# Kernel tuning notes

Measured on AMD Instinct MI355X. Metric: run time of the kernel, lower is better.

The kernel has to match this reference:

```python
import jax, jax.numpy as jnp
import numpy as np

D_MODEL = 1024
NUM_HEADS = 16
D_K = D_MODEL // NUM_HEADS


def setup_inputs() -> dict:
    key = jax.random.key(0)
    ks = jax.random.split(key, 11)
    B, T = 4, 2048
    s = 1.0 / np.sqrt(D_MODEL)
    inp = {
        "query": jax.random.normal(ks[0], (B, T, D_MODEL), jnp.float32),
        "key": jax.random.normal(ks[1], (B, T, D_MODEL), jnp.float32),
        "value": jax.random.normal(ks[2], (B, T, D_MODEL), jnp.float32),
        "Wq": jax.random.uniform(ks[3], (D_MODEL, D_MODEL), jnp.float32, -s, s),
        "bq": jax.random.uniform(ks[4], (D_MODEL,), jnp.float32, -s, s),
        "Wk": jax.random.uniform(ks[5], (D_MODEL, D_MODEL), jnp.float32, -s, s),
        "bk": jax.random.uniform(ks[6], (D_MODEL,), jnp.float32, -s, s),
        "Wv": jax.random.uniform(ks[7], (D_MODEL, D_MODEL), jnp.float32, -s, s),
        "bv": jax.random.uniform(ks[8], (D_MODEL,), jnp.float32, -s, s),
        "Wo": jax.random.uniform(ks[9], (D_MODEL, D_MODEL), jnp.float32, -s, s),
        "bo": jax.random.uniform(ks[10], (D_MODEL,), jnp.float32, -s, s),
    }
    return inp


def _split_heads(x):
    B, T, _ = x.shape
    return x.reshape(B, T, NUM_HEADS, D_K).transpose(0, 2, 1, 3)  # (B,H,T,dk)


def reference(query, key, value, Wq, bq, Wk, bk, Wv, bv, Wo, bo):
    q = _split_heads(query @ Wq + bq)   # (B,H,Tq,dk)
    k = _split_heads(key @ Wk + bk)     # (B,H,Tk,dk)
    v = _split_heads(value @ Wv + bv)   # (B,H,Tk,dk)
    scale = 1.0 / jnp.sqrt(jnp.asarray(D_K, q.dtype))
    scores = jnp.einsum("bhqd,bhkd->bhqk", q, k) * scale
    weights = jax.nn.softmax(scores, axis=-1)
    attn = jnp.einsum("bhqk,bhkd->bhqd", weights, v)  # (B,H,Tq,dk)
    B, H, T, dk = attn.shape
    attn = attn.transpose(0, 2, 1, 3).reshape(B, T, H * dk)
    return attn @ Wo + bo
```

## Files before the change

### kernel.cpp

```cpp
#include <hip/hip_runtime.h>
#include <hip/hip_bf16.h>
#include <stdint.h>


typedef __bf16 bf16x8 __attribute__((ext_vector_type(8)));
typedef float  f32x4  __attribute__((ext_vector_type(4)));

#define LOG2E 1.44269504088896340736f

static __device__ __forceinline__ uint32_t f2bf(float x) {
  uint32_t u = __float_as_uint(x);
  u += 0x7fffu + ((u >> 16) & 1u);
  return u >> 16;
}
#if __has_builtin(__builtin_amdgcn_cvt_pk_bf16_f32)
static __device__ __forceinline__ uint32_t pk2bf(float a, float b) {
  typedef __bf16 b2 __attribute__((ext_vector_type(2)));
  union { b2 v; uint32_t u; } x;
  x.v = __builtin_amdgcn_cvt_pk_bf16_f32(a, b);
  return x.u;
}
#else
static __device__ __forceinline__ uint32_t pk2bf(float a, float b) {
  return f2bf(a) | (f2bf(b) << 16);
}
#endif
static __device__ __forceinline__ void gl2lds16(const void* g, void* l) {
  __builtin_amdgcn_global_load_lds(
      (const __attribute__((address_space(1))) uint32_t*)g,
      (__attribute__((address_space(3))) uint32_t*)l, 16, 0, 0);
}

__global__ void transpose_weights(const float* __restrict__ Wq, const float* __restrict__ Wk,
                                  const float* __restrict__ Wv, const float* __restrict__ Wo,
                                  uint16_t* __restrict__ out) {
  __shared__ float t[32][33];
  const float* W = blockIdx.z == 0 ? Wq : blockIdx.z == 1 ? Wk : blockIdx.z == 2 ? Wv : Wo;
  uint16_t* O = out + (size_t)blockIdx.z * 1048576;
  int tx = threadIdx.x & 31, ty = threadIdx.x >> 5;
  int r0 = blockIdx.y * 32, c0 = blockIdx.x * 32;
#pragma unroll
  for (int i = 0; i < 4; i++) t[ty + i * 8][tx] = W[(size_t)(r0 + ty + i * 8) * 1024 + c0 + tx];
  __syncthreads();
#pragma unroll
  for (int i = 0; i < 4; i++)
    O[(size_t)(c0 + ty + i * 8) * 1024 + r0 + tx] = (uint16_t)f2bf(t[tx][ty + i * 8]);
}

template <bool AF32>
static __device__ __forceinline__ void gemm_body(
    const void* __restrict__ Ain, const uint16_t* __restrict__ Bt,
    const float* __restrict__ bias, void* __restrict__ Cout,
    int N, int K, int mode, float oscale, int mBase, int nBase,
    uint16_t* __restrict__ lA, uint16_t* __restrict__ lB) {
  int tid = threadIdx.x, wave = tid >> 6, lane = tid & 63;
  int q = lane >> 4, c = lane & 15;
  int wrow = wave & 1, wcol = wave >> 1;
  f32x4 acc[4][4] = {};

  int rho = lane >> 3, j = lane & 7;
  int swz = (j ^ rho) * 8;
  const uint16_t* gB  = Bt + (size_t)(nBase + wave * 32 + rho) * K + swz;
  const uint16_t* gA16 = (const uint16_t*)Ain + (size_t)(mBase + wave * 32 + rho) * K + swz;
  const float*    gA32 = (const float*)Ain + (size_t)(mBase + wave * 32 + rho) * K + swz;
  int cs = c & 7;

  for (int kt = 0; kt < K / 64; kt++) {
    __syncthreads();
    int k0 = kt * 64;
#pragma unroll
    for (int it = 0; it < 4; it++)
      gl2lds16(gB + (size_t)(it * 8) * K + k0, &lB[(wave * 32 + it * 8) * 64]);
    if (AF32) {
#pragma unroll
      for (int h2 = 0; h2 < 2; h2++) {
        float4 fa[2][2];
#pragma unroll
        for (int it = 0; it < 2; it++) {
          const float* p = gA32 + (size_t)((h2 * 2 + it) * 8) * K + k0;
          fa[it][0] = *(const float4*)p;
          fa[it][1] = *(const float4*)(p + 4);
        }
#pragma unroll
        for (int it = 0; it < 2; it++) {
          uint4 ov;
          ov.x = pk2bf(fa[it][0].x, fa[it][0].y);
          ov.y = pk2bf(fa[it][0].z, fa[it][0].w);
          ov.z = pk2bf(fa[it][1].x, fa[it][1].y);
          ov.w = pk2bf(fa[it][1].z, fa[it][1].w);
          *(uint4*)&lA[(wave * 32 + (h2 * 2 + it) * 8 + rho) * 64 + j * 8] = ov;
        }
      }
    } else {
#pragma unroll
      for (int it = 0; it < 4; it++)
        gl2lds16(gA16 + (size_t)(it * 8) * K + k0, &lA[(wave * 32 + it * 8) * 64]);
    }
    __syncthreads();
#pragma unroll
    for (int kk = 0; kk < 2; kk++) {
      bf16x8 af[4], bfr[4];
#pragma unroll
      for (int i = 0; i < 4; i++)
        af[i] = *(const bf16x8*)&lA[(wrow * 64 + i * 16 + c) * 64 + ((kk * 4 + q) ^ cs) * 8];
#pragma unroll
      for (int jj = 0; jj < 4; jj++)
        bfr[jj] = *(const bf16x8*)&lB[(wcol * 64 + jj * 16 + c) * 64 + ((kk * 4 + q) ^ cs) * 8];
#pragma unroll
      for (int i = 0; i < 4; i++)
#pragma unroll
        for (int jj = 0; jj < 4; jj++)
          acc[i][jj] = __builtin_amdgcn_mfma_f32_16x16x32_bf16(af[i], bfr[jj], acc[i][jj], 0, 0, 0);
    }
  }

  float bb[4];
#pragma unroll
  for (int jj = 0; jj < 4; jj++) bb[jj] = bias[nBase + wcol * 64 + jj * 16 + c];

  if (mode == 0) {
    float* Co = (float*)Cout;
#pragma unroll
    for (int i = 0; i < 4; i++)
#pragma unroll
      for (int jj = 0; jj < 4; jj++) {
        int row = mBase + wrow * 64 + i * 16 + q * 4;
        int col = nBase + wcol * 64 + jj * 16 + c;
#pragma unroll
        for (int r = 0; r < 4; r++) Co[(size_t)(row + r) * N + col] = acc[i][jj][r] + bb[jj];
      }
  } else if (mode == 1) {
    uint16_t* Co = (uint16_t*)Cout;
#pragma unroll
    for (int i = 0; i < 4; i++)
#pragma unroll
      for (int jj = 0; jj < 4; jj++) {
        int row = mBase + wrow * 64 + i * 16 + q * 4;
        int col = nBase + wcol * 64 + jj * 16 + c;
#pragma unroll
        for (int r = 0; r < 4; r++)
          Co[(size_t)(row + r) * N + col] = (uint16_t)f2bf((acc[i][jj][r] + bb[jj]) * oscale);
      }
  } else {
    uint16_t* Co = (uint16_t*)Cout;
#pragma unroll
    for (int i = 0; i < 4; i++)
#pragma unroll
      for (int jj = 0; jj < 4; jj++) {
        int n = nBase + wcol * 64 + jj * 16 + c;
        int h = n >> 6, d = n & 63;
        int m = mBase + wrow * 64 + i * 16 + q * 4;
        int b = m >> 11, t = m & 2047;
        uint32_t lo = pk2bf(acc[i][jj][0] + bb[jj], acc[i][jj][1] + bb[jj]);
        uint32_t hi = pk2bf(acc[i][jj][2] + bb[jj], acc[i][jj][3] + bb[jj]);
        *(uint2*)(Co + (size_t)((b * 16 + h) * 64 + d) * 2048 + t) = make_uint2(lo, hi);
      }
  }
}

__global__ __launch_bounds__(256, 2)
void gemm_qkv(const float* __restrict__ qs, const float* __restrict__ ks,
              const float* __restrict__ vs, const uint16_t* __restrict__ Wtq,
              const uint16_t* __restrict__ Wtk, const uint16_t* __restrict__ Wtv,
              const float* __restrict__ bq, const float* __restrict__ bk,
              const float* __restrict__ bv, uint16_t* __restrict__ Qp,
              uint16_t* __restrict__ Kp, uint16_t* __restrict__ Vt, float cs) {
  __shared__ uint16_t lA[8192], lB[8192];
  int id = blockIdx.x + (blockIdx.y << 3) + (blockIdx.z << 9);
  int xcd = id & 7, j = id >> 3;
  int bx = j & 7;
  int by = xcd * 8 + ((j >> 3) & 7);
  int z  = j >> 6;
  const void* A      = z == 0 ? (const void*)qs : (z == 1 ? (const void*)ks : (const void*)vs);
  const uint16_t* Bt = z == 0 ? Wtq : (z == 1 ? Wtk : Wtv);
  const float* bias  = z == 0 ? bq : (z == 1 ? bk : bv);
  void* C            = z == 0 ? (void*)Qp : (z == 1 ? (void*)Kp : (void*)Vt);
  int mode   = z == 2 ? 2 : 1;
  float os   = z == 0 ? cs : 1.0f;
  gemm_body<true>(A, Bt, bias, C, 1024, 1024, mode, os, by * 128, bx * 128, lA, lB);
}

__global__ __launch_bounds__(256, 2)
void gemm_out(const uint16_t* __restrict__ A, const uint16_t* __restrict__ Bt,
              const float* __restrict__ bias, float* __restrict__ C) {
  __shared__ uint16_t lA[8192], lB[8192];
  int id = blockIdx.x + (blockIdx.y << 3);
  int xcd = id & 7, j = id >> 3;
  int bx = j & 7;
  int by = xcd * 8 + (j >> 3);
  gemm_body<false>(A, Bt, bias, C, 1024, 1024, 0, 1.0f, by * 128, bx * 128, lA, lB);
}

__global__ __launch_bounds__(256, 2)
void attn(const uint16_t* __restrict__ Qp, const uint16_t* __restrict__ Kp,
          const uint16_t* __restrict__ Vt, uint16_t* __restrict__ Ob) {
  __shared__ uint16_t lds[16384];
  int tid = threadIdx.x, wave = tid >> 6, lane = tid & 63;
  int q = lane >> 4, c = lane & 15;
  int cs = c & 7;
  int gq   = (c & 3) | (((c >> 2) & 1) << 2);
  int rowA = ((c >> 2) << 3) + (c & 3);

  int id = blockIdx.y * 16 + blockIdx.x;
  int wk = (id & 7) * 128 + (id >> 3);
  int qt = wk & 15, bh = wk >> 4;
  int b = bh >> 4, h = bh & 15;
  int qbase = qt * 128;
  int swz = ((lane & 7) ^ (lane >> 3)) * 8;

  {
    const uint16_t* gQ =
        Qp + (size_t)(b * 2048 + qbase + wave * 32 + (lane >> 3)) * 1024 + h * 64 + swz;
#pragma unroll
    for (int it = 0; it < 4; it++)
      gl2lds16(gQ + (size_t)(it * 8) * 1024, &lds[(wave * 32 + it * 8) * 64]);
  }
  __syncthreads();
  bf16x8 qf[2][2];
#pragma unroll
  for (int it = 0; it < 2; it++)
#pragma unroll
    for (int kk = 0; kk < 2; kk++)
      qf[it][kk] =
          *(const bf16x8*)&lds[(wave * 32 + it * 16 + c) * 64 + ((kk * 4 + q) ^ cs) * 8];
  __syncthreads();

  f32x4 o[4][2] = {};
  f32x4 lacc[2] = {};
  union { uint32_t u[4]; bf16x8 v; } one8;
  one8.u[0] = one8.u[1] = one8.u[2] = one8.u[3] = 0x3F803F80u;

  int kchunk = (lane & 7) ^ ((lane >> 3) & 3);
  const uint16_t* gKa =
      Kp + (size_t)(b * 2048 + wave * 16 + (lane >> 3)) * 1024 + h * 64 + kchunk * 8;
  const uint16_t* gKb =
      Kp + (size_t)(b * 2048 + wave * 16 + 8 + (lane >> 3)) * 1024 + h * 64 + (kchunk ^ 4) * 8;
  const uint16_t* gV0 = Vt + (size_t)(bh * 64 + wave * 16 + (lane >> 3)) * 2048 + swz;

  auto stage = [&](int tile, int nb) {
    gl2lds16(gKa + (size_t)(tile * 64) * 1024, &lds[nb + (wave * 16) * 64]);
    gl2lds16(gKb + (size_t)(tile * 64) * 1024, &lds[nb + (wave * 16 + 8) * 64]);
    gl2lds16(gV0 + (size_t)(tile * 64), &lds[8192 + nb + (wave * 16) * 64]);
    gl2lds16(gV0 + (size_t)(8 * 2048) + tile * 64, &lds[8192 + nb + (wave * 16 + 8) * 64]);
  };

  auto compute = [&](const uint16_t* sKc, const uint16_t* sVc) {
    f32x4 s[2][2][2];
#pragma unroll
    for (int p = 0; p < 2; p++) {
      const uint16_t* kr = &sKc[(p * 32 + rowA) * 64];
      bf16x8 aA0 = *(const bf16x8*)&kr[(q ^ gq) * 8];
      bf16x8 aA1 = *(const bf16x8*)&kr[((4 + q) ^ gq) * 8];
      bf16x8 aB0 = *(const bf16x8*)&kr[256 + (q ^ gq) * 8];
      bf16x8 aB1 = *(const bf16x8*)&kr[256 + ((4 + q) ^ gq) * 8];
      s[p][0][0] = __builtin_amdgcn_mfma_f32_16x16x32_bf16(aA0, qf[0][0],
                                                           (f32x4){0.f, 0.f, 0.f, 0.f}, 0, 0, 0);
      s[p][0][0] = __builtin_amdgcn_mfma_f32_16x16x32_bf16(aA1, qf[0][1], s[p][0][0], 0, 0, 0);
      s[p][0][1] = __builtin_amdgcn_mfma_f32_16x16x32_bf16(aA0, qf[1][0],
                                                           (f32x4){0.f, 0.f, 0.f, 0.f}, 0, 0, 0);
      s[p][0][1] = __builtin_amdgcn_mfma_f32_16x16x32_bf16(aA1, qf[1][1], s[p][0][1], 0, 0, 0);
      s[p][1][0] = __builtin_amdgcn_mfma_f32_16x16x32_bf16(aB0, qf[0][0],
                                                           (f32x4){0.f, 0.f, 0.f, 0.f}, 0, 0, 0);
      s[p][1][0] = __builtin_amdgcn_mfma_f32_16x16x32_bf16(aB1, qf[0][1], s[p][1][0], 0, 0, 0);
      s[p][1][1] = __builtin_amdgcn_mfma_f32_16x16x32_bf16(aB0, qf[1][0],
                                                           (f32x4){0.f, 0.f, 0.f, 0.f}, 0, 0, 0);
      s[p][1][1] = __builtin_amdgcn_mfma_f32_16x16x32_bf16(aB1, qf[1][1], s[p][1][1], 0, 0, 0);
    }
#pragma unroll
    for (int p = 0; p < 2; p++) {
      union { uint32_t u[4]; bf16x8 v; } pb[2];
#pragma unroll
      for (int it = 0; it < 2; it++) {
        float a0 = __builtin_amdgcn_exp2f(s[p][0][it][0]);
        float a1 = __builtin_amdgcn_exp2f(s[p][0][it][1]);
        float a2 = __builtin_amdgcn_exp2f(s[p][0][it][2]);
        float a3 = __builtin_amdgcn_exp2f(s[p][0][it][3]);
        float b0 = __builtin_amdgcn_exp2f(s[p][1][it][0]);
        float b1 = __builtin_amdgcn_exp2f(s[p][1][it][1]);
        float b2 = __builtin_amdgcn_exp2f(s[p][1][it][2]);
        float b3 = __builtin_amdgcn_exp2f(s[p][1][it][3]);
        pb[it].u[0] = pk2bf(a0, a1); pb[it].u[1] = pk2bf(a2, a3);
        pb[it].u[2] = pk2bf(b0, b1); pb[it].u[3] = pk2bf(b2, b3);
      }
      lacc[0] = __builtin_amdgcn_mfma_f32_16x16x32_bf16(one8.v, pb[0].v, lacc[0], 0, 0, 0);
      lacc[1] = __builtin_amdgcn_mfma_f32_16x16x32_bf16(one8.v, pb[1].v, lacc[1], 0, 0, 0);
#pragma unroll
      for (int mt = 0; mt < 4; mt++) {
        bf16x8 vv = *(const bf16x8*)&sVc[(mt * 16 + c) * 64 + (((p * 4 + q) ^ cs) * 8)];
        o[mt][0] = __builtin_amdgcn_mfma_f32_16x16x32_bf16(vv, pb[0].v, o[mt][0], 0, 0, 0);
        o[mt][1] = __builtin_amdgcn_mfma_f32_16x16x32_bf16(vv, pb[1].v, o[mt][1], 0, 0, 0);
      }
    }
  };

  stage(0, 0);
  for (int kt2 = 0; kt2 < 16; kt2++) {
    __syncthreads();
    stage(kt2 * 2 + 1, 4096);
    compute(&lds[0], &lds[8192]);
    __syncthreads();
    if (kt2 < 15) stage(kt2 * 2 + 2, 0);
    compute(&lds[4096], &lds[12288]);
  }

  float l[2] = {lacc[0][0], lacc[1][0]};

#pragma unroll
  for (int it = 0; it < 2; it++) {
    float inv = 1.0f / l[it];
    size_t trow = (size_t)(b * 2048 + qbase + wave * 32 + it * 16 + c) * 1024 + h * 64;
#pragma unroll
    for (int mt = 0; mt < 4; mt++) {
      uint32_t lo = pk2bf(o[mt][it][0] * inv, o[mt][it][1] * inv);
      uint32_t hi = pk2bf(o[mt][it][2] * inv, o[mt][it][3] * inv);
      *(uint2*)(Ob + trow + mt * 16 + q * 4) = make_uint2(lo, hi);
    }
  }
}

extern "C" void kernel_launch(void* const* d_in, const int* in_sizes, int n_in,
                              void* d_out, int out_size, void* d_ws, size_t ws_size,
                              hipStream_t stream) {
  (void)in_sizes; (void)n_in; (void)out_size; (void)ws_size;
  const float* query = (const float*)d_in[0];
  const float* key_  = (const float*)d_in[1];
  const float* value = (const float*)d_in[2];
  const float* Wq = (const float*)d_in[3]; const float* bq = (const float*)d_in[4];
  const float* Wk = (const float*)d_in[5]; const float* bk = (const float*)d_in[6];
  const float* Wv = (const float*)d_in[7]; const float* bv = (const float*)d_in[8];
  const float* Wo = (const float*)d_in[9]; const float* bo = (const float*)d_in[10];

  const size_t SZ = (size_t)8192 * 1024;
  uint16_t* buf0 = (uint16_t*)d_ws;
  uint16_t* buf1 = buf0 + SZ;
  uint16_t* buf2 = buf1 + SZ;
  uint16_t* buf3 = buf2 + SZ;
  uint16_t* wts  = buf3 + SZ;
  uint16_t* Wtq = wts;
  uint16_t* Wtk = wts + 1048576;
  uint16_t* Wtv = wts + 2097152;
  uint16_t* Wto = wts + 3145728;
  uint16_t* Kp  = wts + 4194304;
  uint16_t* Vt  = Kp + SZ;

  const float Cs = 0.125f * LOG2E;

  transpose_weights<<<dim3(32, 32, 4), 256, 0, stream>>>(Wq, Wk, Wv, Wo, wts);
  gemm_qkv<<<dim3(8, 64, 3), 256, 0, stream>>>(query, key_, value, Wtq, Wtk, Wtv,
                                               bq, bk, bv, buf3, Kp, Vt, Cs);
  attn<<<dim3(16, 64), 256, 0, stream>>>(buf3, Kp, Vt, buf2);
  gemm_out<<<dim3(8, 64), 256, 0, stream>>>(buf2, Wto, bo, (float*)d_out);
}
```

Baseline: 372.7 us.

## Double-buffer GEMM LDS tiles to overlap global loads with MFMA compute

Reworks the shared GEMM main loop into a two-stage ping-pong pipeline. The next K-tile's global loads (direct-to-LDS for bf16, register-staged for fp32 with bf16 conversion) are issued before computing on the current buffer, which hides load latency behind MFMA work. LDS per block doubles to 64 KB, and more fp32 staging registers stay live, both of which may reduce occupancy. The loop now hardcodes K/64 = 16 iterations.

```diff
diff --git a/kernel.cpp b/kernel.cpp
--- a/kernel.cpp
+++ b/kernel.cpp
@@ -60,58 +60,76 @@
 
   int rho = lane >> 3, j = lane & 7;
   int swz = (j ^ rho) * 8;
-  const uint16_t* gB  = Bt + (size_t)(nBase + wave * 32 + rho) * K + swz;
+  const uint16_t* gB   = Bt + (size_t)(nBase + wave * 32 + rho) * K + swz;
   const uint16_t* gA16 = (const uint16_t*)Ain + (size_t)(mBase + wave * 32 + rho) * K + swz;
   const float*    gA32 = (const float*)Ain + (size_t)(mBase + wave * 32 + rho) * K + swz;
   int cs = c & 7;
 
-  for (int kt = 0; kt < K / 64; kt++) {
-    __syncthreads();
-    int k0 = kt * 64;
+  float4 fa[4][2];
+
+  auto issueA32 = [&](int kt) {
+#pragma unroll
+    for (int it = 0; it < 4; it++) {
+      const float* p = gA32 + (size_t)(it * 8) * K + kt * 64;
+      fa[it][0] = *(const float4*)p;
+      fa[it][1] = *(const float4*)(p + 4);
+    }
+  };
+  auto writeA32 = [&](int nb) {
+#pragma unroll
+    for (int it = 0; it < 4; it++) {
+      uint4 ov;
+      ov.x = pk2bf(fa[it][0].x, fa[it][0].y);
+      ov.y = pk2bf(fa[it][0].z, fa[it][0].w);
+      ov.z = pk2bf(fa[it][1].x, fa[it][1].y);
+      ov.w = pk2bf(fa[it][1].z, fa[it][1].w);
+      *(uint4*)&lA[nb + (wave * 32 + it * 8 + rho) * 64 + j * 8] = ov;
+    }
+  };
+  auto issueA16 = [&](int kt, int nb) {
 #pragma unroll
     for (int it = 0; it < 4; it++)
-      gl2lds16(gB + (size_t)(it * 8) * K + k0, &lB[(wave * 32 + it * 8) * 64]);
-    if (AF32) {
-#pragma unroll
-      for (int h2 = 0; h2 < 2; h2++) {
-        float4 fa[2][2];
-#pragma unroll
-        for (int it = 0; it < 2; it++) {
-          const float* p = gA32 + (size_t)((h2 * 2 + it) * 8) * K + k0;
-          fa[it][0] = *(const float4*)p;
-          fa[it][1] = *(const float4*)(p + 4);
-        }
-#pragma unroll
-        for (int it = 0; it < 2; it++) {
-          uint4 ov;
-          ov.x = pk2bf(fa[it][0].x, fa[it][0].y);
-          ov.y = pk2bf(fa[it][0].z, fa[it][0].w);
-          ov.z = pk2bf(fa[it][1].x, fa[it][1].y);
-          ov.w = pk2bf(fa[it][1].z, fa[it][1].w);
-          *(uint4*)&lA[(wave * 32 + (h2 * 2 + it) * 8 + rho) * 64 + j * 8] = ov;
-        }
-      }
-    } else {
-#pragma unroll
-      for (int it = 0; it < 4; it++)
-        gl2lds16(gA16 + (size_t)(it * 8) * K + k0, &lA[(wave * 32 + it * 8) * 64]);
-    }
-    __syncthreads();
+      gl2lds16(gA16 + (size_t)(it * 8) * K + kt * 64, &lA[nb + (wave * 32 + it * 8) * 64]);
+  };
+  auto issueB = [&](int kt, int nb) {
+#pragma unroll
+    for (int it = 0; it < 4; it++)
+      gl2lds16(gB + (size_t)(it * 8) * K + kt * 64, &lB[nb + (wave * 32 + it * 8) * 64]);
+  };
+  auto compute = [&](int nb) {
 #pragma unroll
     for (int kk = 0; kk < 2; kk++) {
       bf16x8 af[4], bfr[4];
 #pragma unroll
       for (int i = 0; i < 4; i++)
-        af[i] = *(const bf16x8*)&lA[(wrow * 64 + i * 16 + c) * 64 + ((kk * 4 + q) ^ cs) * 8];
+        af[i] = *(const bf16x8*)&lA[nb + (wrow * 64 + i * 16 + c) * 64 + ((kk * 4 + q) ^ cs) * 8];
 #pragma unroll
       for (int jj = 0; jj < 4; jj++)
-        bfr[jj] = *(const bf16x8*)&lB[(wcol * 64 + jj * 16 + c) * 64 + ((kk * 4 + q) ^ cs) * 8];
+        bfr[jj] = *(const bf16x8*)&lB[nb + (wcol * 64 + jj * 16 + c) * 64 + ((kk * 4 + q) ^ cs) * 8];
 #pragma unroll
       for (int i = 0; i < 4; i++)
 #pragma unroll
         for (int jj = 0; jj < 4; jj++)
           acc[i][jj] = __builtin_amdgcn_mfma_f32_16x16x32_bf16(af[i], bfr[jj], acc[i][jj], 0, 0, 0);
     }
+  };
+
+  if (AF32) { issueA32(0); writeA32(0); } else issueA16(0, 0);
+  issueB(0, 0);
+
+  for (int kt2 = 0; kt2 < 8; kt2++) {
+    __syncthreads();
+    if (AF32) issueA32(kt2 * 2 + 1); else issueA16(kt2 * 2 + 1, 8192);
+    issueB(kt2 * 2 + 1, 8192);
+    compute(0);
+    if (AF32) writeA32(8192);
+    __syncthreads();
+    if (kt2 < 7) {
+      if (AF32) issueA32(kt2 * 2 + 2); else issueA16(kt2 * 2 + 2, 0);
+      issueB(kt2 * 2 + 2, 0);
+    }
+    compute(8192);
+    if (AF32 && kt2 < 7) writeA32(0);
   }
 
   float bb[4];
@@ -165,7 +183,7 @@
               const float* __restrict__ bq, const float* __restrict__ bk,
               const float* __restrict__ bv, uint16_t* __restrict__ Qp,
               uint16_t* __restrict__ Kp, uint16_t* __restrict__ Vt, float cs) {
-  __shared__ uint16_t lA[8192], lB[8192];
+  __shared__ uint16_t lA[16384], lB[16384];
   int id = blockIdx.x + (blockIdx.y << 3) + (blockIdx.z << 9);
   int xcd = id & 7, j = id >> 3;
   int bx = j & 7;
@@ -183,7 +201,7 @@
 __global__ __launch_bounds__(256, 2)
 void gemm_out(const uint16_t* __restrict__ A, const uint16_t* __restrict__ Bt,
               const float* __restrict__ bias, float* __restrict__ C) {
-  __shared__ uint16_t lA[8192], lB[8192];
+  __shared__ uint16_t lA[16384], lB[16384];
   int id = blockIdx.x + (blockIdx.y << 3);
   int xcd = id & 7, j = id >> 3;
   int bx = j & 7;
```

Result: faster. 350.2 us (-6.0%).
